# Kernel tuning notes

Hardware: AMD Instinct MI355X
Metric: run time of the kernel (lower is better)

The kernel has to match this reference:

```python
import jax, jax.numpy as jnp
import numpy as np

N = 200000   # nodes (all node types share one set here)
E = 1000000  # edges per graph meta-path
D = 64       # in_size == out_size * layer_num_heads (8*8)
H = 128      # semantic attention hidden size


def setup_inputs() -> dict:
    key = jax.random.key(0)
    ks = jax.random.split(key, 16)
    s = 0.05
    return {
        "h": jax.random.normal(ks[0], (N, D), jnp.float32),
        "src1": jax.random.randint(ks[1], (E,), 0, N, jnp.int32),
        "dst1": jax.random.randint(ks[2], (E,), 0, N, jnp.int32),
        "src2": jax.random.randint(ks[3], (E,), 0, N, jnp.int32),
        "dst2": jax.random.randint(ks[4], (E,), 0, N, jnp.int32),
        "W_id": jax.random.normal(ks[5], (D, D), jnp.float32) * s,
        "b_id": jnp.zeros((D,), jnp.float32),
        "W1": jax.random.normal(ks[6], (D, D), jnp.float32) * s,
        "b1": jnp.zeros((D,), jnp.float32),
        "W2": jax.random.normal(ks[7], (D, D), jnp.float32) * s,
        "b2": jnp.zeros((D,), jnp.float32),
        "Wp1": jax.random.normal(ks[8], (D, H), jnp.float32) * s,
        "bp1": jnp.zeros((H,), jnp.float32),
        "Wp2": jax.random.normal(ks[9], (H, 1), jnp.float32) * s,
    }


def _right_norm_edge_weights(dst):
    # adj_norm='right': weight = 1 / in_degree(dst), nan/inf -> 0
    deg = jax.ops.segment_sum(jnp.ones((E,), jnp.float32), dst, num_segments=N)
    inv = jnp.where(deg > 0, 1.0 / deg, 0.0)
    return inv[dst]  # [E]


def _mean_agg(h, src, dst, W, b):
    # MeanAggregator, eval mode (dropout off), in_feats == out_feats:
    # aggregate (u_mul_e + sum) first, then project, bias, ELU.
    ew = _right_norm_edge_weights(dst)                       # [E]
    msg = h[src] * ew[:, None]                               # [E, D] gather-mul
    agg = jax.ops.segment_sum(msg, dst, num_segments=N)      # [N, D] scatter-add
    return jax.nn.elu(agg @ W + b)


def _semantic_attention(z, Wp1, bp1, Wp2):
    # z: [N, P, D]
    w = (jnp.tanh(z @ Wp1 + bp1) @ Wp2).mean(0)              # [P, 1]
    beta = jax.nn.softmax(w, axis=0)                         # [P, 1]
    return (beta[None, :, :] * z).sum(1)                     # [N, D]


def reference(h, src1, dst1, src2, dst2, W_id, b_id, W1, b1, W2, b2, Wp1, bp1, Wp2):
    ident = h @ W_id + b_id                                  # len-1 meta-path: Linear only
    e1 = _mean_agg(h, src1, dst1, W1, b1)
    e2 = _mean_agg(h, src2, dst2, W2, b2)
    z = jnp.stack([ident, e1, e2], axis=1)                   # [N, 3, D]
    return _semantic_attention(z, Wp1, bp1, Wp2)
```

## Files before the change

kernel.cpp:

```cpp
#include <hip/hip_runtime.h>
#include <math.h>

#define DD 64
#define HH 128
#define SCHUNK 2048

typedef __attribute__((ext_vector_type(8))) short bf16x8;
typedef __attribute__((ext_vector_type(4))) short s16x4;
typedef __attribute__((ext_vector_type(4))) float f32x4;
typedef __attribute__((ext_vector_type(4))) int i32x4;

__device__ __forceinline__ short f2bf(float x){
    unsigned u = __builtin_bit_cast(unsigned, x);
    u += 0x7fffu + ((u >> 16) & 1u);
    return (short)(u >> 16);
}
__device__ __forceinline__ float bf2f(short s){
    unsigned u = ((unsigned)(unsigned short)s) << 16;
    return __builtin_bit_cast(float, u);
}
__device__ __forceinline__ float fast_tanh(float x){
    float e = __expf(2.0f * x);
    return 1.0f - 2.0f / (e + 1.0f);
}
__device__ __forceinline__ float elu1(float x){
    return x > 0.0f ? x : (__expf(x) - 1.0f);
}

__global__ __launch_bounds__(256) void hist_conv(
    const int* __restrict__ dst1, const int* __restrict__ dst2,
    const float* __restrict__ h,
    int* __restrict__ cnt1, int* __restrict__ cnt2,
    short* __restrict__ h_bf, int E, int Nq) {
    int tid = blockIdx.x * 256 + threadIdx.x;
    if (tid < E) {
        atomicAdd(&cnt1[dst1[tid]], 1);
        atomicAdd(&cnt2[dst2[tid]], 1);
    }
    if (tid < Nq) {
        float4 v = ((const float4*)h)[tid];
        s16x4 o;
        o[0] = f2bf(v.x); o[1] = f2bf(v.y); o[2] = f2bf(v.z); o[3] = f2bf(v.w);
        ((s16x4*)h_bf)[tid] = o;
    }
}

__global__ __launch_bounds__(256) void scan_reduce(
    const int* __restrict__ c1, const int* __restrict__ c2,
    int* __restrict__ part, int n, int nch) {
    int b = blockIdx.x;
    int g = b >= nch;
    const int* cnt = g ? c2 : c1;
    int cb = b - g * nch;
    int n4 = n >> 2;
    int i4 = cb * (SCHUNK / 4) + threadIdx.x * 2;
    int s = 0;
    #pragma unroll
    for (int k = 0; k < 2; k++) {
        if (i4 + k < n4) {
            int4 v = ((const int4*)cnt)[i4 + k];
            s += v.x + v.y + v.z + v.w;
        }
    }
    #pragma unroll
    for (int off = 32; off >= 1; off >>= 1) s += __shfl_xor(s, off, 64);
    __shared__ int red[4];
    int wv = threadIdx.x >> 6;
    if ((threadIdx.x & 63) == 0) red[wv] = s;
    __syncthreads();
    if (threadIdx.x == 0) part[b] = red[0] + red[1] + red[2] + red[3];
}

__global__ void scan_mid(int* __restrict__ part, int nch) {
    int t = threadIdx.x;
    if (t < 2) {
        int* p = part + t * nch;
        int run = 0;
        for (int i = 0; i < nch; i++) { int v = p[i]; p[i] = run; run += v; }
    }
}

__global__ __launch_bounds__(256) void scan_final(
    const int* __restrict__ c1, int* __restrict__ o1,
    const int* __restrict__ c2, int* __restrict__ o2,
    const int* __restrict__ part, int n, int nch) {
    int b = blockIdx.x;
    int g = b >= nch;
    const int* cnt = g ? c2 : c1;
    int* off       = g ? o2 : o1;
    int cb = b - g * nch;
    int n4 = n >> 2;
    int i4 = cb * (SCHUNK / 4) + threadIdx.x * 2;
    int4 v0 = {0,0,0,0}, v1 = {0,0,0,0};
    if (i4 < n4)     v0 = ((const int4*)cnt)[i4];
    if (i4 + 1 < n4) v1 = ((const int4*)cnt)[i4 + 1];
    int s = v0.x+v0.y+v0.z+v0.w + v1.x+v1.y+v1.z+v1.w;

    __shared__ int ssum[256];
    int tid = threadIdx.x;
    ssum[tid] = s;
    __syncthreads();
    for (int d = 1; d < 256; d <<= 1) {
        int t = (tid >= d) ? ssum[tid - d] : 0;
        __syncthreads();
        ssum[tid] += t;
        __syncthreads();
    }
    int run = part[b] + ssum[tid] - s;

    int4 o0, o1v;
    o0.x = run; run += v0.x;
    o0.y = run; run += v0.y;
    o0.z = run; run += v0.z;
    o0.w = run; run += v0.w;
    o1v.x = run; run += v1.x;
    o1v.y = run; run += v1.y;
    o1v.z = run; run += v1.z;
    o1v.w = run; run += v1.w;
    if (i4 < n4)     ((int4*)off)[i4]     = o0;
    if (i4 + 1 < n4) ((int4*)off)[i4 + 1] = o1v;
}

__global__ __launch_bounds__(256) void esort(
    const int* __restrict__ src1, const int* __restrict__ dst1,
    const int* __restrict__ src2, const int* __restrict__ dst2,
    int* __restrict__ off1, int* __restrict__ off2,
    int* __restrict__ eidx1, int* __restrict__ eidx2, int E) {
    int e = blockIdx.x * 256 + threadIdx.x;
    if (e >= E) return;
    { int d = dst1[e]; int pos = atomicAdd(&off1[d], 1); eidx1[pos] = src1[e]; }
    { int d = dst2[e]; int pos = atomicAdd(&off2[d], 1); eidx2[pos] = src2[e]; }
}

__global__ __launch_bounds__(256) void gather(
    const float* __restrict__ h,
    const int* __restrict__ cnt1, const int* __restrict__ off1,
    const int* __restrict__ eidx1, short* __restrict__ a1bf,
    const int* __restrict__ cnt2, const int* __restrict__ off2,
    const int* __restrict__ eidx2, short* __restrict__ a2bf, int N) {
    int w = blockIdx.x * 4 + (threadIdx.x >> 6);
    int lane = threadIdx.x & 63;
    if (w >= 2 * N) return;
    int g = w >= N;
    int n = g ? w - N : w;
    const int* cnt  = g ? cnt2  : cnt1;
    const int* off  = g ? off2  : off1;
    const int* eidx = g ? eidx2 : eidx1;
    short* abf      = g ? a2bf  : a1bf;

    int end = off[n];
    int deg = cnt[n];
    int i = end - deg;
    float acc = 0.f;
    for (; i + 1 < end; i += 2) {
        int s0 = eidx[i], s1 = eidx[i + 1];
        float v0 = h[(size_t)s0 * DD + lane];
        float v1 = h[(size_t)s1 * DD + lane];
        acc += v0 + v1;
    }
    if (i < end) acc += h[(size_t)eidx[i] * DD + lane];
    float inv = deg > 0 ? 1.f / (float)deg : 0.f;
    abf[(size_t)n * DD + lane] = f2bf(acc * inv);
}

__global__ __launch_bounds__(256, 2) void fuse_kernel(
    const short* __restrict__ h_bf,
    const float* __restrict__ W_id, const float* __restrict__ b_id,
    const float* __restrict__ W1, const float* __restrict__ b1,
    const float* __restrict__ W2, const float* __restrict__ b2,
    const float* __restrict__ Wp1, const float* __restrict__ bp1,
    const float* __restrict__ Wp2,
    const short* __restrict__ a1bf, const short* __restrict__ a2bf,
    short* __restrict__ zbuf1, short* __restrict__ zbuf2,
    float* __restrict__ w_acc, int N)
{
    __shared__ __align__(16) short sWb[12288];
    __shared__ __align__(16) short sWp[8192];
    __shared__ __align__(16) short sZ[4][3072];

    for (int i = threadIdx.x; i < 12288; i += 256) {
        int p = i >> 12, r = i & 4095;
        int ct = r >> 10, rr = r & 1023;
        int ks = rr >> 9, q = rr & 511;
        int ln = q >> 3, j = q & 7;
        int c = ct * 16 + (ln & 15);
        int k = ks * 32 + (ln >> 4) * 8 + j;
        int idx = k * DD + c;
        float v = (p == 0) ? W_id[idx] : (p == 1 ? W1[idx] : W2[idx]);
        sWb[i] = f2bf(v);
    }
    for (int i = threadIdx.x; i < 8192; i += 256) {
        int ct = i >> 10, rr = i & 1023;
        int ks = rr >> 9, q = rr & 511;
        int ln = q >> 3, j = q & 7;
        int c = ct * 16 + (ln & 15);
        int k = ks * 32 + (ln >> 4) * 8 + j;
        sWp[i] = f2bf(Wp1[k * HH + c]);
    }

    int lane = threadIdx.x & 63;
    int wv = threadIdx.x >> 6;
    int cl = lane & 15;
    int quad = lane >> 4;

    float bid[4], bb1r[4], bb2r[4];
    #pragma unroll
    for (int ct = 0; ct < 4; ct++) {
        bid[ct]  = b_id[ct*16 + cl];
        bb1r[ct] = b1[ct*16 + cl];
        bb2r[ct] = b2[ct*16 + cl];
    }
    float bpr[8], wp2r[8];
    #pragma unroll
    for (int ct = 0; ct < 8; ct++) {
        bpr[ct]  = bp1[ct*16 + cl];
        wp2r[ct] = Wp2[ct*16 + cl];
    }
    __syncthreads();

    float wsp0 = 0.f, wsp1 = 0.f, wsp2 = 0.f;
    int ntiles = (N + 63) >> 6;
    short* zw = sZ[wv];

    for (int tile = blockIdx.x; tile < ntiles; tile += gridDim.x) {
        int nb = tile * 64 + wv * 16;
        int arow = nb + cl;
        int arowc = arow < N ? arow : N - 1;

        f32x4 acc[3][4];
        #pragma unroll
        for (int p = 0; p < 3; p++)
            #pragma unroll
            for (int ct = 0; ct < 4; ct++)
                acc[p][ct] = (f32x4){0.f,0.f,0.f,0.f};

        #pragma unroll
        for (int ks = 0; ks < 2; ks++) {
            int kb = ks*32 + quad*8;
            bf16x8 fa0 = *(const bf16x8*)&h_bf[(size_t)arowc*DD + kb];
            bf16x8 fa1 = *(const bf16x8*)&a1bf[(size_t)arowc*DD + kb];
            bf16x8 fa2 = *(const bf16x8*)&a2bf[(size_t)arowc*DD + kb];
            #pragma unroll
            for (int ct = 0; ct < 4; ct++) {
                bf16x8 w0 = *(const bf16x8*)&sWb[        (ct*2+ks)*512 + lane*8];
                bf16x8 w1 = *(const bf16x8*)&sWb[4096 +  (ct*2+ks)*512 + lane*8];
                bf16x8 w2 = *(const bf16x8*)&sWb[8192 +  (ct*2+ks)*512 + lane*8];
                acc[0][ct] = __builtin_amdgcn_mfma_f32_16x16x32_bf16(fa0, w0, acc[0][ct], 0,0,0);
                acc[1][ct] = __builtin_amdgcn_mfma_f32_16x16x32_bf16(fa1, w1, acc[1][ct], 0,0,0);
                acc[2][ct] = __builtin_amdgcn_mfma_f32_16x16x32_bf16(fa2, w2, acc[2][ct], 0,0,0);
            }
        }

        #pragma unroll
        for (int ct = 0; ct < 4; ct++) {
            int c = ct*16 + cl;
            int obase = (c >> 5)*512 + ((c >> 3) & 3)*128 + (c & 7);
            #pragma unroll
            for (int r = 0; r < 4; r++) {
                int m = quad*4 + r;
                int off = obase + m*8;
                float z0 = acc[0][ct][r] + bid[ct];
                float z1 = elu1(acc[1][ct][r] + bb1r[ct]);
                float z2 = elu1(acc[2][ct][r] + bb2r[ct]);
                zw[off]        = f2bf(z0);
                zw[1024 + off] = f2bf(z1);
                zw[2048 + off] = f2bf(z2);
            }
        }

        float rmask[4];
        #pragma unroll
        for (int r = 0; r < 4; r++)
            rmask[r] = (nb + quad*4 + r) < N ? 1.f : 0.f;

        #pragma unroll
        for (int p = 0; p < 3; p++) {
            bf16x8 zA = *(const bf16x8*)&zw[p*1024 +       lane*8];
            bf16x8 zB = *(const bf16x8*)&zw[p*1024 + 512 + lane*8];
            float wsum = 0.f;
            #pragma unroll
            for (int ct = 0; ct < 8; ct++) {
                f32x4 t = (f32x4){0.f,0.f,0.f,0.f};
                bf16x8 u0 = *(const bf16x8*)&sWp[(ct*2+0)*512 + lane*8];
                bf16x8 u1 = *(const bf16x8*)&sWp[(ct*2+1)*512 + lane*8];
                t = __builtin_amdgcn_mfma_f32_16x16x32_bf16(zA, u0, t, 0,0,0);
                t = __builtin_amdgcn_mfma_f32_16x16x32_bf16(zB, u1, t, 0,0,0);
                float s = 0.f;
                #pragma unroll
                for (int r = 0; r < 4; r++)
                    s += fast_tanh(t[r] + bpr[ct]) * rmask[r];
                wsum += s * wp2r[ct];
            }
            if (p == 0)      wsp0 += wsum;
            else if (p == 1) wsp1 += wsum;
            else             wsp2 += wsum;
        }

        int m8 = lane >> 3;
        int q3 = lane & 7;
        int ks2 = q3 >> 2, qq = q3 & 3;
        #pragma unroll
        for (int pass = 0; pass < 2; pass++) {
            int m = pass*8 + m8;
            int node = nb + m;
            if (node < N) {
                int lo = ks2*512 + (m + qq*16)*8;
                i32x4 v0 = *(const i32x4*)&zw[lo];
                i32x4 v1 = *(const i32x4*)&zw[1024 + lo];
                i32x4 v2 = *(const i32x4*)&zw[2048 + lo];
                char* base1 = (char*)zbuf1 + (size_t)node*256 + ks2*64 + qq*16;
                *(i32x4*)base1 = v1;
                *(i32x4*)(base1 + 128) = v0;
                char* base2 = (char*)zbuf2 + (size_t)node*128 + ks2*64 + qq*16;
                *(i32x4*)base2 = v2;
            }
        }
    }

    #pragma unroll
    for (int off = 32; off >= 1; off >>= 1) {
        wsp0 += __shfl_xor(wsp0, off, 64);
        wsp1 += __shfl_xor(wsp1, off, 64);
        wsp2 += __shfl_xor(wsp2, off, 64);
    }
    if (lane == 0) {
        atomicAdd(&w_acc[0], wsp0);
        atomicAdd(&w_acc[1], wsp1);
        atomicAdd(&w_acc[2], wsp2);
    }
}

__global__ __launch_bounds__(256) void out_kernel(
    const short* __restrict__ zbuf1, const short* __restrict__ zbuf2,
    const float* __restrict__ w_acc, float* __restrict__ out,
    int N, float invN)
{
    int tid = blockIdx.x * 256 + threadIdx.x;
    int n = tid >> 3, part = tid & 7;
    if (n >= N) return;
    float w0 = w_acc[0]*invN, w1 = w_acc[1]*invN, w2 = w_acc[2]*invN;
    float m = fmaxf(w0, fmaxf(w1, w2));
    float e0 = __expf(w0-m), e1 = __expf(w1-m), e2 = __expf(w2-m);
    float s = 1.f/(e0+e1+e2);
    float beta0 = e0*s, beta1 = e1*s, beta2 = e2*s;

    const char* r1 = (const char*)zbuf1 + (size_t)n*256 + part*16;
    const char* r2 = (const char*)zbuf2 + (size_t)n*128 + part*16;
    union U { i32x4 v; short sh[8]; };
    U z1u, z0u, z2u;
    z1u.v = *(const i32x4*)r1;
    z0u.v = *(const i32x4*)(r1 + 128);
    z2u.v = *(const i32x4*)r2;
    float tmp[8];
    #pragma unroll
    for (int j = 0; j < 8; j++)
        tmp[j] = beta0*bf2f(z0u.sh[j]) + beta1*bf2f(z1u.sh[j]) + beta2*bf2f(z2u.sh[j]);
    float4* op = (float4*)(out + (size_t)n*64 + part*8);
    op[0] = (float4){tmp[0],tmp[1],tmp[2],tmp[3]};
    op[1] = (float4){tmp[4],tmp[5],tmp[6],tmp[7]};
}

extern "C" void kernel_launch(void* const* d_in, const int* in_sizes, int n_in,
                              void* d_out, int out_size, void* d_ws, size_t ws_size,
                              hipStream_t stream) {
    const float* h    = (const float*)d_in[0];
    const int*   src1 = (const int*)d_in[1];
    const int*   dst1 = (const int*)d_in[2];
    const int*   src2 = (const int*)d_in[3];
    const int*   dst2 = (const int*)d_in[4];
    const float* W_id = (const float*)d_in[5];
    const float* b_id = (const float*)d_in[6];
    const float* W1   = (const float*)d_in[7];
    const float* b1   = (const float*)d_in[8];
    const float* W2   = (const float*)d_in[9];
    const float* b2   = (const float*)d_in[10];
    const float* Wp1  = (const float*)d_in[11];
    const float* bp1  = (const float*)d_in[12];
    const float* Wp2  = (const float*)d_in[13];
    float* out = (float*)d_out;

    int N = in_sizes[0] / DD;
    int E = in_sizes[1];
    int nch = (N + SCHUNK - 1) / SCHUNK;

    char* p = (char*)d_ws;
    int*   cnt1  = (int*)p;   p += (size_t)N * 4;
    int*   cnt2  = (int*)p;   p += (size_t)N * 4;
    float* w_acc = (float*)p; p += 32;
    int*   part  = (int*)p;   p += (size_t)2 * nch * 4;
    int*   off1  = (int*)p;   p += (size_t)N * 4;
    int*   off2  = (int*)p;   p += (size_t)N * 4;
    int*   eidx1 = (int*)p;   p += (size_t)E * 4;
    int*   eidx2 = (int*)p;   p += (size_t)E * 4;
    short* h_bf  = (short*)p; p += (size_t)N * DD * 2;
    short* a1bf  = (short*)p; p += (size_t)N * DD * 2;
    short* a2bf  = (short*)p; p += (size_t)N * DD * 2;
    short* zbuf1 = (short*)p; p += (size_t)N * 128 * 2;
    short* zbuf2 = (short*)p; p += (size_t)N * DD * 2;

    hipMemsetAsync(d_ws, 0, (size_t)2 * N * 4 + 32, stream);

    int Nq = N * 16;
    int hc_threads = Nq > E ? Nq : E;
    hist_conv<<<(hc_threads + 255) / 256, 256, 0, stream>>>(
        dst1, dst2, h, cnt1, cnt2, h_bf, E, Nq);

    scan_reduce<<<2 * nch, 256, 0, stream>>>(cnt1, cnt2, part, N, nch);
    scan_mid<<<1, 64, 0, stream>>>(part, nch);
    scan_final<<<2 * nch, 256, 0, stream>>>(cnt1, off1, cnt2, off2, part, N, nch);

    esort<<<(E + 255) / 256, 256, 0, stream>>>(
        src1, dst1, src2, dst2, off1, off2, eidx1, eidx2, E);

    gather<<<(2 * N + 3) / 4, 256, 0, stream>>>(
        h, cnt1, off1, eidx1, a1bf, cnt2, off2, eidx2, a2bf, N);

    int ntiles = (N + 63) >> 6;
    int fblocks = ntiles < 512 ? ntiles : 512;
    fuse_kernel<<<fblocks, 256, 0, stream>>>(h_bf, W_id, b_id, W1, b1, W2, b2,
                                             Wp1, bp1, Wp2, a1bf, a2bf,
                                             zbuf1, zbuf2, w_acc, N);

    out_kernel<<<(N * 8 + 255) / 256, 256, 0, stream>>>(zbuf1, zbuf2, w_acc, out, N, 1.0f / (float)N);
}
```

Baseline: 675.2 us.

## Replace per-edge atomic sort and per-node gather with bucketed binsort and LDS aggregation

The per-edge global-atomic counting sort is replaced by a two-level bucket sort. Each block histograms a chunk of edges into 256-node buckets in shared memory, reserves global space per bucket with one atomic, stages the edges in LDS, and writes them out contiguously. Each edge is packed as the source index plus the low 8 bits of the destination. Aggregation then runs one block per bucket, accumulating neighbour rows read from the bf16 copy of h into a 64 KB LDS accumulator with shared float atomics, instead of one wave per node reading fp32 rows. This aims to cut random global atomics, scattered writes and gather bandwidth, at the cost of bf16 input precision, nondeterministic summation order and a 1024-bucket cap.

```diff
diff --git a/kernel.cpp b/kernel.cpp
--- a/kernel.cpp
+++ b/kernel.cpp
@@ -4,6 +4,7 @@
 #define DD 64
 #define HH 128
 #define SCHUNK 2048
+#define BCHUNK 8192
 
 typedef __attribute__((ext_vector_type(8))) short bf16x8;
 typedef __attribute__((ext_vector_type(4))) short s16x4;
@@ -121,46 +122,142 @@
     if (i4 + 1 < n4) ((int4*)off)[i4 + 1] = o1v;
 }
 
-__global__ __launch_bounds__(256) void esort(
+__global__ __launch_bounds__(256) void bucket_init(
+    const int* __restrict__ off1, const int* __restrict__ off2,
+    int* __restrict__ bcur1, int* __restrict__ bcur2, int NB) {
+    int b = blockIdx.x * 256 + threadIdx.x;
+    if (b < NB) {
+        bcur1[b] = off1[b << 8];
+        bcur2[b] = off2[b << 8];
+    }
+}
+
+__global__ __launch_bounds__(256) void binsort(
     const int* __restrict__ src1, const int* __restrict__ dst1,
     const int* __restrict__ src2, const int* __restrict__ dst2,
-    int* __restrict__ off1, int* __restrict__ off2,
-    int* __restrict__ eidx1, int* __restrict__ eidx2, int E) {
-    int e = blockIdx.x * 256 + threadIdx.x;
-    if (e >= E) return;
-    { int d = dst1[e]; int pos = atomicAdd(&off1[d], 1); eidx1[pos] = src1[e]; }
-    { int d = dst2[e]; int pos = atomicAdd(&off2[d], 1); eidx2[pos] = src2[e]; }
-}
-
-__global__ __launch_bounds__(256) void gather(
-    const float* __restrict__ h,
+    int* __restrict__ bcur1, int* __restrict__ bcur2,
+    unsigned* __restrict__ ebuf1, unsigned* __restrict__ ebuf2,
+    int E, int nch)
+{
+    __shared__ int sHist[1024];
+    __shared__ int sBase[1025];
+    __shared__ int sGb[1024];
+    __shared__ unsigned sStage[BCHUNK];
+    __shared__ int sTS[256];
+
+    int bc = blockIdx.x;
+    int g = bc >= nch;
+    int chunk = bc - g * nch;
+    const int* src = g ? src2 : src1;
+    const int* dst = g ? dst2 : dst1;
+    int* bcur      = g ? bcur2 : bcur1;
+    unsigned* ebuf = g ? ebuf2 : ebuf1;
+    int e0 = chunk * BCHUNK;
+    int elen = E - e0; if (elen > BCHUNK) elen = BCHUNK;
+
+    int tid = threadIdx.x;
+    for (int i = tid; i < 1024; i += 256) sHist[i] = 0;
+    __syncthreads();
+    for (int j = tid; j < elen; j += 256)
+        atomicAdd(&sHist[dst[e0 + j] >> 8], 1);
+    __syncthreads();
+
+    int a0 = sHist[4*tid], a1 = sHist[4*tid+1], a2 = sHist[4*tid+2], a3 = sHist[4*tid+3];
+    int s = a0 + a1 + a2 + a3;
+    sTS[tid] = s;
+    __syncthreads();
+    for (int d = 1; d < 256; d <<= 1) {
+        int t = (tid >= d) ? sTS[tid - d] : 0;
+        __syncthreads();
+        sTS[tid] += t;
+        __syncthreads();
+    }
+    int run = sTS[tid] - s;
+    sBase[4*tid]   = run; run += a0;
+    sBase[4*tid+1] = run; run += a1;
+    sBase[4*tid+2] = run; run += a2;
+    sBase[4*tid+3] = run; run += a3;
+    if (tid == 255) sBase[1024] = run;
+    __syncthreads();
+
+    for (int b = tid; b < 1024; b += 256) {
+        int cnt = sBase[b+1] - sBase[b];
+        sHist[b] = 0;
+        if (cnt > 0) sGb[b] = atomicAdd(&bcur[b], cnt);
+    }
+    __syncthreads();
+
+    for (int j = tid; j < elen; j += 256) {
+        int d = dst[e0 + j];
+        int sr = src[e0 + j];
+        int b = d >> 8;
+        int pos = atomicAdd(&sHist[b], 1);
+        sStage[sBase[b] + pos] = ((unsigned)sr << 8) | (unsigned)(d & 255);
+    }
+    __syncthreads();
+
+    int wv = tid >> 6, lane = tid & 63;
+    for (int b = wv; b < 1024; b += 4) {
+        int cnt = sBase[b+1] - sBase[b];
+        if (cnt <= 0) continue;
+        int gb = sGb[b], sb = sBase[b];
+        for (int j = lane; j < cnt; j += 64)
+            ebuf[gb + j] = sStage[sb + j];
+    }
+}
+
+__global__ __launch_bounds__(256) void agg(
+    const short* __restrict__ h_bf,
     const int* __restrict__ cnt1, const int* __restrict__ off1,
-    const int* __restrict__ eidx1, short* __restrict__ a1bf,
+    const unsigned* __restrict__ ebuf1, short* __restrict__ a1bf,
     const int* __restrict__ cnt2, const int* __restrict__ off2,
-    const int* __restrict__ eidx2, short* __restrict__ a2bf, int N) {
-    int w = blockIdx.x * 4 + (threadIdx.x >> 6);
-    int lane = threadIdx.x & 63;
-    if (w >= 2 * N) return;
-    int g = w >= N;
-    int n = g ? w - N : w;
-    const int* cnt  = g ? cnt2  : cnt1;
-    const int* off  = g ? off2  : off1;
-    const int* eidx = g ? eidx2 : eidx1;
-    short* abf      = g ? a2bf  : a1bf;
-
-    int end = off[n];
-    int deg = cnt[n];
-    int i = end - deg;
-    float acc = 0.f;
-    for (; i + 1 < end; i += 2) {
-        int s0 = eidx[i], s1 = eidx[i + 1];
-        float v0 = h[(size_t)s0 * DD + lane];
-        float v1 = h[(size_t)s1 * DD + lane];
-        acc += v0 + v1;
-    }
-    if (i < end) acc += h[(size_t)eidx[i] * DD + lane];
-    float inv = deg > 0 ? 1.f / (float)deg : 0.f;
-    abf[(size_t)n * DD + lane] = f2bf(acc * inv);
+    const unsigned* __restrict__ ebuf2, short* __restrict__ a2bf,
+    int N, int NB, int E)
+{
+    __shared__ float sAcc[256 * DD];
+    int bid = blockIdx.x;
+    int g = bid >= NB;
+    int sb = bid - g * NB;
+    const int* cnt       = g ? cnt2  : cnt1;
+    const int* off       = g ? off2  : off1;
+    const unsigned* ebuf = g ? ebuf2 : ebuf1;
+    short* abf           = g ? a2bf  : a1bf;
+
+    int tid = threadIdx.x;
+    for (int i = tid; i < 256 * DD; i += 256) sAcc[i] = 0.f;
+
+    int start = off[sb << 8];
+    int nodeEnd = (sb + 1) << 8;
+    int end = nodeEnd >= N ? E : off[nodeEnd];
+    __syncthreads();
+
+    int wv = tid >> 6, lane = tid & 63;
+    int half = lane >> 5, hl = lane & 31;
+    for (int e = start + wv * 2 + half; e < end; e += 8) {
+        unsigned v = ebuf[e];
+        int dl = v & 255;
+        int sr = v >> 8;
+        unsigned hw = ((const unsigned*)h_bf)[(size_t)sr * 32 + hl];
+        float f0 = bf2f((short)(hw & 0xffff));
+        float f1 = bf2f((short)(hw >> 16));
+        atomicAdd(&sAcc[dl * DD + hl * 2],     f0);
+        atomicAdd(&sAcc[dl * DD + hl * 2 + 1], f1);
+    }
+    __syncthreads();
+
+    for (int k = 0; k < 32; k++) {
+        int nl = wv * 64 + k * 2 + half;
+        int node = (sb << 8) + nl;
+        if (node < N) {
+            int dg = cnt[node];
+            float inv = dg > 0 ? 1.f / (float)dg : 0.f;
+            float f0 = sAcc[nl * DD + hl * 2] * inv;
+            float f1 = sAcc[nl * DD + hl * 2 + 1] * inv;
+            unsigned o = (unsigned)(unsigned short)f2bf(f0)
+                       | ((unsigned)(unsigned short)f2bf(f1) << 16);
+            ((unsigned*)abf)[(size_t)node * 32 + hl] = o;
+        }
+    }
 }
 
 __global__ __launch_bounds__(256, 2) void fuse_kernel(
@@ -382,6 +479,7 @@
     int N = in_sizes[0] / DD;
     int E = in_sizes[1];
     int nch = (N + SCHUNK - 1) / SCHUNK;
+    int NB  = (N + 255) >> 8;
 
     char* p = (char*)d_ws;
     int*   cnt1  = (int*)p;   p += (size_t)N * 4;
@@ -390,8 +488,10 @@
     int*   part  = (int*)p;   p += (size_t)2 * nch * 4;
     int*   off1  = (int*)p;   p += (size_t)N * 4;
     int*   off2  = (int*)p;   p += (size_t)N * 4;
-    int*   eidx1 = (int*)p;   p += (size_t)E * 4;
-    int*   eidx2 = (int*)p;   p += (size_t)E * 4;
+    int*   bcur1 = (int*)p;   p += (size_t)1024 * 4;
+    int*   bcur2 = (int*)p;   p += (size_t)1024 * 4;
+    unsigned* ebuf1 = (unsigned*)p; p += (size_t)E * 4;
+    unsigned* ebuf2 = (unsigned*)p; p += (size_t)E * 4;
     short* h_bf  = (short*)p; p += (size_t)N * DD * 2;
     short* a1bf  = (short*)p; p += (size_t)N * DD * 2;
     short* a2bf  = (short*)p; p += (size_t)N * DD * 2;
@@ -409,11 +509,15 @@
     scan_mid<<<1, 64, 0, stream>>>(part, nch);
     scan_final<<<2 * nch, 256, 0, stream>>>(cnt1, off1, cnt2, off2, part, N, nch);
 
-    esort<<<(E + 255) / 256, 256, 0, stream>>>(
-        src1, dst1, src2, dst2, off1, off2, eidx1, eidx2, E);
-
-    gather<<<(2 * N + 3) / 4, 256, 0, stream>>>(
-        h, cnt1, off1, eidx1, a1bf, cnt2, off2, eidx2, a2bf, N);
+    bucket_init<<<(NB + 255) / 256, 256, 0, stream>>>(off1, off2, bcur1, bcur2, NB);
+
+    int nech = (E + BCHUNK - 1) / BCHUNK;
+    binsort<<<2 * nech, 256, 0, stream>>>(src1, dst1, src2, dst2,
+                                          bcur1, bcur2, ebuf1, ebuf2, E, nech);
+
+    agg<<<2 * NB, 256, 0, stream>>>(h_bf,
+                                    cnt1, off1, ebuf1, a1bf,
+                                    cnt2, off2, ebuf2, a2bf, N, NB, E);
 
     int ntiles = (N + 63) >> 6;
     int fblocks = ntiles < 512 ? ntiles : 512;
```

Measured after the change: 1.175 ms. +74.0%, slower.
